# Performance work log

Hardware: AMD Instinct MI355X
Metric: run time of the kernel (lower is better)

The kernel has to match this reference:

```python
import jax, jax.numpy as jnp
import numpy as np

B, S, HID = 2, 2048, 2048
H, KV, D = 16, 8, 128          # query heads, kv heads, head_dim
EPS = 1e-6
THETA = 1000000.0


def setup_inputs() -> dict:
    key = jax.random.key(0)
    ks = jax.random.split(key, 8)
    sc = 0.02
    hidden_states = jax.random.normal(ks[0], (B, S, HID), dtype=jnp.float32)
    Wq = jax.random.normal(ks[1], (HID, H * D), dtype=jnp.float32) * sc
    Wk = jax.random.normal(ks[2], (HID, KV * D), dtype=jnp.float32) * sc
    Wv = jax.random.normal(ks[3], (HID, KV * D), dtype=jnp.float32) * sc
    Wo = jax.random.normal(ks[4], (H * D, HID), dtype=jnp.float32) * sc
    q_norm_w = jnp.ones((D,), dtype=jnp.float32)
    k_norm_w = jnp.ones((D,), dtype=jnp.float32)
    positions = jnp.arange(S, dtype=jnp.int32)
    # causal mask: True = masked (j > i)
    attention_mask = jnp.triu(jnp.ones((S, S), dtype=bool), k=1)
    return {
        "hidden_states": hidden_states, "Wq": Wq, "Wk": Wk, "Wv": Wv,
        "Wo": Wo, "q_norm_w": q_norm_w, "k_norm_w": k_norm_w,
        "positions": positions, "attention_mask": attention_mask,
    }


def _rms_norm(x, w):
    # x: [..., D]; RMSNorm over last dim
    var = jnp.mean(x * x, axis=-1, keepdims=True)
    return x * jax.lax.rsqrt(var + EPS) * w


def _rope(x, positions):
    # x: [B, h, S, D]; standard rotate-half RoPE
    inv_freq = 1.0 / (THETA ** (jnp.arange(0, D, 2, dtype=jnp.float32) / D))
    ang = positions.astype(jnp.float32)[:, None] * inv_freq[None, :]  # [S, D/2]
    cos = jnp.concatenate([jnp.cos(ang), jnp.cos(ang)], axis=-1)      # [S, D]
    sin = jnp.concatenate([jnp.sin(ang), jnp.sin(ang)], axis=-1)
    x1, x2 = x[..., : D // 2], x[..., D // 2:]
    rot = jnp.concatenate([-x2, x1], axis=-1)
    return x * cos + rot * sin


def reference(hidden_states, Wq, Wk, Wv, Wo, q_norm_w, k_norm_w,
              positions, attention_mask):
    b, s, _ = hidden_states.shape
    q = (hidden_states @ Wq).reshape(b, s, H, D).transpose(0, 2, 1, 3)   # [B,H,S,D]
    k = (hidden_states @ Wk).reshape(b, s, KV, D).transpose(0, 2, 1, 3)  # [B,KV,S,D]
    v = (hidden_states @ Wv).reshape(b, s, KV, D).transpose(0, 2, 1, 3)
    q = _rms_norm(q, q_norm_w)
    k = _rms_norm(k, k_norm_w)
    q = _rope(q, positions)
    k = _rope(k, positions)
    # GQA: repeat kv heads
    g = H // KV
    k = jnp.repeat(k, g, axis=1)  # [B,H,S,D]
    v = jnp.repeat(v, g, axis=1)
    scale = 1.0 / np.sqrt(D).astype(np.float32)
    scores = jnp.einsum('bhqd,bhkd->bhqk', q, k) * scale
    scores = jnp.where(attention_mask[None, None, :, :], -jnp.inf, scores)
    attn = jax.nn.softmax(scores, axis=-1)
    out = jnp.einsum('bhqk,bhkd->bhqd', attn, v)
    out = out.transpose(0, 2, 1, 3).reshape(b, s, H * D)
    return out @ Wo
```

## Files before the change

kernel.cpp:

```cpp
#include <hip/hip_runtime.h>
#include <hip/hip_bf16.h>

typedef __hip_bfloat16 bf16;
typedef __attribute__((ext_vector_type(8))) short short8v;
typedef __attribute__((ext_vector_type(4))) float f32x4;

constexpr int nB = 2;
constexpr int nS = 2048;
constexpr int nHID = 2048;
constexpr int nH = 16;
constexpr int nKV = 8;
constexpr int nD = 128;
constexpr int QS = 4096;
constexpr float kEps = 1e-6f;
constexpr float kScale = 0.08838834764831845f;

template <int N>
struct IC {
  static constexpr int value = N;
};

__device__ inline float b2f(unsigned short u) {
  return __uint_as_float(((unsigned)u) << 16);
}
__device__ inline float bf2f(bf16 v) { return __bfloat162float(v); }
__device__ inline short f2bs(float f) {
  bf16 h = __float2bfloat16(f);
  return *reinterpret_cast<short*>(&h);
}
__device__ inline unsigned pack2bf(float a, float b) {
  return ((unsigned)(unsigned short)f2bs(b) << 16) |
         (unsigned)(unsigned short)f2bs(a);
}

__device__ inline void gload_lds16(const bf16* g, bf16* l) {
  __builtin_amdgcn_global_load_lds(
      (const __attribute__((address_space(1))) void*)g,
      (__attribute__((address_space(3))) void*)l, 16, 0, 0);
}

template <int N>
__device__ inline void vwait() {
  asm volatile("s_waitcnt vmcnt(%0)" ::"n"(N) : "memory");
}

__global__ __launch_bounds__(256) void cvt_f32_bf16(
    const float* __restrict__ src, bf16* __restrict__ dst, int n) {
  const int i = (blockIdx.x * 256 + threadIdx.x) * 4;
  if (i >= n) return;
  const float4 v = *reinterpret_cast<const float4*>(src + i);
  ushort4 o;
  o.x = (unsigned short)f2bs(v.x);
  o.y = (unsigned short)f2bs(v.y);
  o.z = (unsigned short)f2bs(v.z);
  o.w = (unsigned short)f2bs(v.w);
  *reinterpret_cast<ushort4*>(dst + i) = o;
}

__global__ __launch_bounds__(64) void rope_table(float2* __restrict__ tab) {
  const int s = blockIdx.x, j = threadIdx.x;
  const float invf = expf(-(float)j * (13.815510557964274f / 64.0f));
  const float ang = (float)s * invf;
  tab[s * 64 + j] = make_float2(cosf(ang), sinf(ang));
}

__global__ __launch_bounds__(256) void transpose_f32_bf16(
    const float* __restrict__ src, bf16* __restrict__ dst, int K, int N) {
  __shared__ float t[32][33];
  const int k0 = blockIdx.y * 32, n0 = blockIdx.x * 32;
  const int c = threadIdx.x & 31, r8 = threadIdx.x >> 5;
#pragma unroll
  for (int i = 0; i < 4; ++i)
    t[r8 + i * 8][c] = src[(size_t)(k0 + r8 + i * 8) * N + n0 + c];
  __syncthreads();
#pragma unroll
  for (int i = 0; i < 4; ++i)
    dst[(size_t)(n0 + r8 + i * 8) * K + k0 + c] =
        __float2bfloat16(t[c][r8 + i * 8]);
}

template <int BM, typename OUT_T>
__global__ __launch_bounds__(512) void gemm_8ph(
    const bf16* __restrict__ A, const bf16* __restrict__ Bt,
    OUT_T* __restrict__ C, int M, int N, int K) {
  constexpr int LA = BM / 128;
  constexpr int LB = 2;
  constexpr int MF = BM / 32;
  constexpr int MFH = MF / 2;
  constexpr int W = 2 * (LA + LB);
  constexpr int LDSB = 2 * BM * 32 + 2 * 256 * 32;
  __shared__ bf16 lds[2 * LDSB];

  const int tid = threadIdx.x;
  const int wave = tid >> 6, lane = tid & 63;
  const int lr = lane & 15, lg = lane >> 4;
  const int wm = wave >> 2, wn = wave & 3;
  const int m0 = blockIdx.y * BM, n0 = blockIdx.x * 256;
  const int srow = tid >> 2, scol = (tid & 3) * 8;

  auto stageA = [&](int t, int kk) {
    bf16* dst = lds + (t & 1) * LDSB + kk * (BM * 32) + wave * 512;
    const bf16* src = A + (size_t)(m0 + srow) * K + t * 64 + kk * 32 + scol;
#pragma unroll
    for (int j = 0; j < LA; ++j)
      gload_lds16(src + (size_t)(j * 128) * K, dst + j * 4096);
  };
  auto stageB = [&](int t, int kk) {
    bf16* dst =
        lds + (t & 1) * LDSB + 2 * BM * 32 + kk * (256 * 32) + wave * 512;
    const bf16* src = Bt + (size_t)(n0 + srow) * K + t * 64 + kk * 32 + scol;
#pragma unroll
    for (int j = 0; j < LB; ++j)
      gload_lds16(src + (size_t)(j * 128) * K, dst + j * 4096);
  };

  f32x4 acc[MF][4];
#pragma unroll
  for (int m = 0; m < MF; ++m)
#pragma unroll
    for (int n = 0; n < 4; ++n) acc[m][n] = (f32x4){0.f, 0.f, 0.f, 0.f};
  short8v bfr[4];

  auto phase = [&](auto WC, int buf, int kk, int mh, auto stageFn) {
    constexpr int WAIT = decltype(WC)::value;
    if constexpr (WAIT >= 0) vwait<WAIT>();
    __builtin_amdgcn_s_barrier();
    asm volatile("" ::: "memory");
    if (mh == 0) {
      const bf16* bb = lds + buf * LDSB + 2 * BM * 32 + kk * (256 * 32);
#pragma unroll
      for (int ni = 0; ni < 4; ++ni)
        bfr[ni] = *reinterpret_cast<const short8v*>(
            bb + (wn * 64 + ni * 16 + lr) * 32 + lg * 8);
    }
    short8v af[MFH];
    const bf16* ab = lds + buf * LDSB + kk * (BM * 32);
#pragma unroll
    for (int ii = 0; ii < MFH; ++ii)
      af[ii] = *reinterpret_cast<const short8v*>(
          ab + (wm * (BM / 2) + (mh * MFH + ii) * 16 + lr) * 32 + lg * 8);
    stageFn();
    asm volatile("s_waitcnt lgkmcnt(0)" ::: "memory");
    __builtin_amdgcn_sched_barrier(0);
    __builtin_amdgcn_s_setprio(1);
#pragma unroll
    for (int ii = 0; ii < MFH; ++ii)
#pragma unroll
      for (int ni = 0; ni < 4; ++ni)
        acc[mh * MFH + ii][ni] = __builtin_amdgcn_mfma_f32_16x16x32_bf16(
            af[ii], bfr[ni], acc[mh * MFH + ii][ni], 0, 0, 0);
    __builtin_amdgcn_s_setprio(0);
  };

  const int NT = K / 64;
  stageA(0, 0);
  stageB(0, 0);
  stageA(0, 1);
  stageB(0, 1);
  stageA(1, 0);
  stageB(1, 0);

  for (int t = 0; t < NT - 1; ++t) {
    const int buf = t & 1;
    phase(IC<W>{}, buf, 0, 0, [&] { stageA(t + 1, 1); });
    phase(IC<-1>{}, buf, 0, 1, [&] { stageB(t + 1, 1); });
    phase(IC<W>{}, buf, 1, 0, [&] {
      if (t < NT - 2) stageA(t + 2, 0);
    });
    phase(IC<-1>{}, buf, 1, 1, [&] {
      if (t < NT - 2) stageB(t + 2, 0);
    });
  }
  {
    const int buf = (NT - 1) & 1;
    phase(IC<LA + LB>{}, buf, 0, 0, [&] {});
    phase(IC<-1>{}, buf, 0, 1, [&] {});
    phase(IC<0>{}, buf, 1, 0, [&] {});
    phase(IC<-1>{}, buf, 1, 1, [&] {});
  }

#pragma unroll
  for (int m = 0; m < MF; ++m)
#pragma unroll
    for (int n = 0; n < 4; ++n)
#pragma unroll
      for (int r = 0; r < 4; ++r) {
        const int row = m0 + wm * (BM / 2) + m * 16 + 4 * lg + r;
        const int col = n0 + wn * 64 + n * 16 + lr;
        if constexpr (sizeof(OUT_T) == 2)
          C[(size_t)row * N + col] = __float2bfloat16(acc[m][n][r]);
        else
          C[(size_t)row * N + col] = acc[m][n][r];
      }
}

__global__ __launch_bounds__(128) void norm_rope_fused(
    bf16* __restrict__ qkv, const float* __restrict__ qw,
    const float* __restrict__ kw, const float2* __restrict__ tab) {
  const int row = blockIdx.x;
  const int head = blockIdx.y;
  const int t = threadIdx.x;
  const int s = row & (nS - 1);
  const bool isQ = head < nH;
  const int col = isQ ? head * nD : 2048 + (head - nH) * nD;
  const float* w = isQ ? qw : kw;
  bf16* xp = qkv + (size_t)row * QS + col;
  const float v = bf2f(xp[t]);
  float ss = v * v;
#pragma unroll
  for (int off = 32; off > 0; off >>= 1) ss += __shfl_xor(ss, off);
  __shared__ float wsum[2];
  __shared__ float buf[nD];
  if ((t & 63) == 0) wsum[t >> 6] = ss;
  __syncthreads();
  const float inv = rsqrtf((wsum[0] + wsum[1]) * (1.0f / nD) + kEps);
  const float nv = v * inv * w[t];
  buf[t] = nv;
  __syncthreads();
  const float partner = buf[t ^ 64];
  const float rot = (t < 64) ? -partner : partner;
  const int j = t & 63;
  const float2 cs = tab[s * 64 + j];
  const float outv = nv * cs.x + rot * cs.y;
  xp[t] = __float2bfloat16(outv);
}

constexpr int BQ = 128, BKT = 64;

__global__ __launch_bounds__(512) void attn_mfma(
    const bf16* __restrict__ QKV, bf16* __restrict__ O) {
  const int l = blockIdx.x;
  const int bh = l & 31;
  const int rr0 = l >> 5;
  const int qb = (rr0 < 8) ? 15 - rr0 : rr0 - 8;
  const int b = bh >> 4, h = bh & 15, kvh = h >> 1;
  const int q0 = qb * BQ;
  const int nt = 2 * qb + 2;
  const int tid = threadIdx.x;
  const int wave = tid >> 6, lane = tid & 63;
  const int lr = lane & 15, lg = lane >> 4;

  __shared__ bf16 Ks[BKT][136];
  __shared__ bf16 Vt[nD][72];
  __shared__ bf16 Pl[8][16][72];

  const bf16* Qbase = QKV + (size_t)b * nS * QS + h * nD;
  const bf16* Kbase = QKV + (size_t)b * nS * QS + 2048 + kvh * nD;
  const bf16* Vbase = QKV + (size_t)b * nS * QS + 3072 + kvh * nD;

  const int krow = tid >> 3, kcc = (tid & 7) * 16;
  const int vkey = tid & 63, vdc = (tid >> 6) * 16;

  short8v kreg[2], vreg[2];
  auto gload = [&](int kt) {
    const bf16* ksrc = Kbase + (size_t)(kt + krow) * QS + kcc;
    const bf16* vsrc = Vbase + (size_t)(kt + vkey) * QS + vdc;
    kreg[0] = *reinterpret_cast<const short8v*>(ksrc);
    kreg[1] = *reinterpret_cast<const short8v*>(ksrc + 8);
    vreg[0] = *reinterpret_cast<const short8v*>(vsrc);
    vreg[1] = *reinterpret_cast<const short8v*>(vsrc + 8);
  };
  auto lwrite = [&]() {
    *reinterpret_cast<short8v*>(&Ks[krow][kcc]) = kreg[0];
    *reinterpret_cast<short8v*>(&Ks[krow][kcc + 8]) = kreg[1];
#pragma unroll
    for (int i = 0; i < 2; ++i)
#pragma unroll
      for (int j = 0; j < 8; ++j)
        *reinterpret_cast<short*>(&Vt[vdc + 8 * i + j][vkey]) = vreg[i][j];
  };

  short8v qf[4];
  {
    const bf16* qrow = Qbase + (size_t)(q0 + 16 * wave + lr) * QS;
#pragma unroll
    for (int dc = 0; dc < 4; ++dc)
      qf[dc] = *reinterpret_cast<const short8v*>(qrow + 32 * dc + 8 * lg);
  }

  f32x4 of[8];
#pragma unroll
  for (int n = 0; n < 8; ++n) of[n] = (f32x4){0.f, 0.f, 0.f, 0.f};
  float m_run = -1e30f, l_run = 0.f;

  gload(0);
  lwrite();
  __syncthreads();

  for (int j = 0; j < nt; ++j) {
    const int kt = j * BKT;
    const bool have_next = (j + 1 < nt);
    if (have_next) gload((j + 1) * BKT);

    f32x4 s[4];
    __builtin_amdgcn_s_setprio(1);
#pragma unroll
    for (int sub = 0; sub < 4; ++sub) {
      f32x4 acc = {0.f, 0.f, 0.f, 0.f};
#pragma unroll
      for (int dc = 0; dc < 4; ++dc) {
        const short8v kf = *reinterpret_cast<const short8v*>(
            &Ks[16 * sub + lr][32 * dc + 8 * lg]);
        acc = __builtin_amdgcn_mfma_f32_16x16x32_bf16(kf, qf[dc], acc, 0, 0, 0);
      }
      s[sub] = acc;
    }
    __builtin_amdgcn_s_setprio(0);

    const bool needMask = (kt + BKT > q0 + 16 * wave);
#pragma unroll
    for (int sub = 0; sub < 4; ++sub)
#pragma unroll
      for (int r = 0; r < 4; ++r) {
        float v = s[sub][r] * kScale;
        if (needMask && (kt + 16 * sub + 4 * lg + r > q0 + 16 * wave + lr))
          v = -1e30f;
        s[sub][r] = v;
      }

    float pmax = -1e30f;
#pragma unroll
    for (int sub = 0; sub < 4; ++sub)
#pragma unroll
      for (int r = 0; r < 4; ++r) pmax = fmaxf(pmax, s[sub][r]);
    pmax = fmaxf(pmax, __shfl_xor(pmax, 16));
    pmax = fmaxf(pmax, __shfl_xor(pmax, 32));

    if (!__all(pmax - m_run <= 8.f)) {
      const float mt = fmaxf(m_run, pmax);
      const float corr = __expf(m_run - mt);
#pragma unroll
      for (int n = 0; n < 8; ++n) of[n] *= corr;
      l_run *= corr;
      m_run = mt;
    }

    float p[4][4];
    float lsum = 0.f;
#pragma unroll
    for (int sub = 0; sub < 4; ++sub)
#pragma unroll
      for (int r = 0; r < 4; ++r) {
        const float e = __expf(s[sub][r] - m_run);
        p[sub][r] = e;
        lsum += e;
      }
    lsum += __shfl_xor(lsum, 16);
    lsum += __shfl_xor(lsum, 32);
    l_run += lsum;

#pragma unroll
    for (int sub = 0; sub < 4; ++sub)
#pragma unroll
      for (int rp = 0; rp < 2; ++rp)
        *reinterpret_cast<unsigned*>(
            &Pl[wave][lr][16 * sub + 4 * lg + 2 * rp]) =
            pack2bf(p[sub][2 * rp], p[sub][2 * rp + 1]);

    __builtin_amdgcn_s_setprio(1);
#pragma unroll
    for (int kk = 0; kk < 2; ++kk) {
      const short8v pb =
          *reinterpret_cast<const short8v*>(&Pl[wave][lr][32 * kk + 8 * lg]);
#pragma unroll
      for (int n = 0; n < 8; ++n) {
        const short8v vf = *reinterpret_cast<const short8v*>(
            &Vt[16 * n + lr][32 * kk + 8 * lg]);
        of[n] = __builtin_amdgcn_mfma_f32_16x16x32_bf16(vf, pb, of[n], 0, 0, 0);
      }
    }
    __builtin_amdgcn_s_setprio(0);

    if (have_next) {
      __syncthreads();
      lwrite();
      __syncthreads();
    }
  }

  {
    const float inv = 1.0f / l_run;
    bf16* orow = O + ((size_t)(b * nS + q0 + 16 * wave + lr)) * (nH * nD) +
                 h * nD + 4 * lg;
#pragma unroll
    for (int n = 0; n < 8; ++n)
#pragma unroll
      for (int rp = 0; rp < 2; ++rp)
        *reinterpret_cast<unsigned*>(orow + 16 * n + 2 * rp) =
            pack2bf(of[n][2 * rp] * inv, of[n][2 * rp + 1] * inv);
  }
}

extern "C" void kernel_launch(void* const* d_in, const int* in_sizes, int n_in,
                              void* d_out, int out_size, void* d_ws,
                              size_t ws_size, hipStream_t stream) {
  const float* hs = (const float*)d_in[0];
  const float* Wq = (const float*)d_in[1];
  const float* Wk = (const float*)d_in[2];
  const float* Wv = (const float*)d_in[3];
  const float* Wo = (const float*)d_in[4];
  const float* qw = (const float*)d_in[5];
  const float* kw = (const float*)d_in[6];

  const int M = nB * nS;
  char* ws = (char*)d_ws;
  size_t off = 0;
  auto alloc = [&](size_t bytes) {
    char* p = ws + off;
    off += bytes;
    return p;
  };
  bf16* hsb = (bf16*)alloc((size_t)M * nHID * 2);
  bf16* att = hsb;
  bf16* qkv = (bf16*)alloc((size_t)M * QS * 2);
  bf16* Wcat = (bf16*)alloc((size_t)QS * nHID * 2);
  bf16* Wot = (bf16*)alloc((size_t)nH * nD * nHID * 2);
  float2* tab = (float2*)alloc((size_t)nS * 64 * 8);
  float* out = (float*)d_out;

  const int nHsElems = M * nHID;
  rope_table<<<dim3(nS), 64, 0, stream>>>(tab);
  cvt_f32_bf16<<<(nHsElems / 4 + 255) / 256, 256, 0, stream>>>(hs, hsb,
                                                               nHsElems);
  transpose_f32_bf16<<<dim3(nH * nD / 32, nHID / 32), 256, 0, stream>>>(
      Wq, Wcat, nHID, nH * nD);
  transpose_f32_bf16<<<dim3(nKV * nD / 32, nHID / 32), 256, 0, stream>>>(
      Wk, Wcat + (size_t)2048 * nHID, nHID, nKV * nD);
  transpose_f32_bf16<<<dim3(nKV * nD / 32, nHID / 32), 256, 0, stream>>>(
      Wv, Wcat + (size_t)3072 * nHID, nHID, nKV * nD);
  transpose_f32_bf16<<<dim3(nHID / 32, nH * nD / 32), 256, 0, stream>>>(
      Wo, Wot, nH * nD, nHID);

  gemm_8ph<256, bf16><<<dim3(QS / 256, M / 256), 512, 0, stream>>>(
      hsb, Wcat, qkv, M, QS, nHID);

  norm_rope_fused<<<dim3(M, nH + nKV), 128, 0, stream>>>(qkv, qw, kw, tab);

  attn_mfma<<<dim3(512), 512, 0, stream>>>(qkv, att);

  gemm_8ph<128, float><<<dim3(nHID / 256, M / 128), 512, 0, stream>>>(
      att, Wot, out, M, nHID, nH * nD);
}
```

Before: 261.7 us.

## Double-buffer K via direct global-to-LDS loads with XOR swizzle; merge weight transposes

The attention kernel now stages K tiles straight from global memory into a double-buffered, XOR-swizzled LDS layout (gload_lds16), so K no longer passes through registers and the next tile's load overlaps the current tile's compute. V is loaded as four rows per thread and written transposed with packed 4-element stores instead of scalar shorts. The four weight-transpose launches are merged into one kernel to cut launch overhead. The cost is more LDS for the second K buffer and an extra vmcnt wait before each barrier. Helper functions gload_lds16 and vwait are assumed to exist in the unshown part of the file.

Result: no change. 265.7 us (+1.5%).

```diff
diff --git a/kernel.cpp b/kernel.cpp
--- a/kernel.cpp
+++ b/kernel.cpp
@@ -64,19 +64,35 @@
   tab[s * 64 + j] = make_float2(cosf(ang), sinf(ang));
 }
 
-__global__ __launch_bounds__(256) void transpose_f32_bf16(
-    const float* __restrict__ src, bf16* __restrict__ dst, int K, int N) {
-  __shared__ float t[32][33];
-  const int k0 = blockIdx.y * 32, n0 = blockIdx.x * 32;
+__global__ __launch_bounds__(256) void transpose_all(
+    const float* __restrict__ Wq, const float* __restrict__ Wk,
+    const float* __restrict__ Wv, const float* __restrict__ Wo,
+    bf16* __restrict__ Wcat, bf16* __restrict__ Wot) {
+  int t = blockIdx.x;
+  const float* src;
+  bf16* dst;
+  int N;
+  if (t < 4096) {
+    src = Wq; dst = Wcat; N = 2048;
+  } else if (t < 6144) {
+    t -= 4096; src = Wk; dst = Wcat + (size_t)2048 * 2048; N = 1024;
+  } else if (t < 8192) {
+    t -= 6144; src = Wv; dst = Wcat + (size_t)3072 * 2048; N = 1024;
+  } else {
+    t -= 8192; src = Wo; dst = Wot; N = 2048;
+  }
+  const int tilesN = N >> 5;
+  const int n0 = (t % tilesN) * 32, k0 = (t / tilesN) * 32;
+  __shared__ float tb[32][33];
   const int c = threadIdx.x & 31, r8 = threadIdx.x >> 5;
 #pragma unroll
   for (int i = 0; i < 4; ++i)
-    t[r8 + i * 8][c] = src[(size_t)(k0 + r8 + i * 8) * N + n0 + c];
+    tb[r8 + i * 8][c] = src[(size_t)(k0 + r8 + i * 8) * N + n0 + c];
   __syncthreads();
 #pragma unroll
   for (int i = 0; i < 4; ++i)
-    dst[(size_t)(n0 + r8 + i * 8) * K + k0 + c] =
-        __float2bfloat16(t[c][r8 + i * 8]);
+    dst[(size_t)(n0 + r8 + i * 8) * 2048 + k0 + c] =
+        __float2bfloat16(tb[c][r8 + i * 8]);
 }
 
 template <int BM, typename OUT_T>
@@ -240,7 +256,7 @@
   const int wave = tid >> 6, lane = tid & 63;
   const int lr = lane & 15, lg = lane >> 4;
 
-  __shared__ bf16 Ks[BKT][136];
+  __shared__ bf16 Ks[2][64 * 128];
   __shared__ bf16 Vt[nD][72];
   __shared__ bf16 Pl[8][16][72];
 
@@ -248,26 +264,32 @@
   const bf16* Kbase = QKV + (size_t)b * nS * QS + 2048 + kvh * nD;
   const bf16* Vbase = QKV + (size_t)b * nS * QS + 3072 + kvh * nD;
 
-  const int krow = tid >> 3, kcc = (tid & 7) * 16;
-  const int vkey = tid & 63, vdc = (tid >> 6) * 16;
-
-  short8v kreg[2], vreg[2];
-  auto gload = [&](int kt) {
-    const bf16* ksrc = Kbase + (size_t)(kt + krow) * QS + kcc;
-    const bf16* vsrc = Vbase + (size_t)(kt + vkey) * QS + vdc;
-    kreg[0] = *reinterpret_cast<const short8v*>(ksrc);
-    kreg[1] = *reinterpret_cast<const short8v*>(ksrc + 8);
-    vreg[0] = *reinterpret_cast<const short8v*>(vsrc);
-    vreg[1] = *reinterpret_cast<const short8v*>(vsrc + 8);
-  };
-  auto lwrite = [&]() {
-    *reinterpret_cast<short8v*>(&Ks[krow][kcc]) = kreg[0];
-    *reinterpret_cast<short8v*>(&Ks[krow][kcc + 8]) = kreg[1];
-#pragma unroll
-    for (int i = 0; i < 2; ++i)
-#pragma unroll
-      for (int j = 0; j < 8; ++j)
-        *reinterpret_cast<short*>(&Vt[vdc + 8 * i + j][vkey]) = vreg[i][j];
+  const int kr = tid >> 4;
+  const int ksw = ((tid & 15) ^ (kr & 7)) * 8;
+  auto stageK = [&](int kt, int buf) {
+    const bf16* src = Kbase + (size_t)(kt + kr) * QS + ksw;
+    gload_lds16(src, &Ks[buf][wave * 512]);
+    gload_lds16(src + (size_t)32 * QS, &Ks[buf][4096 + wave * 512]);
+  };
+
+  const int vk = (tid & 15) * 4, vd = (tid >> 4) * 8;
+  short8v vreg[4];
+  auto vload = [&](int kt) {
+    const bf16* src = Vbase + (size_t)(kt + vk) * QS + vd;
+#pragma unroll
+    for (int i = 0; i < 4; ++i)
+      vreg[i] = *reinterpret_cast<const short8v*>(src + (size_t)i * QS);
+  };
+  auto vwrite = [&]() {
+#pragma unroll
+    for (int j = 0; j < 8; ++j) {
+      ushort4 pk;
+      pk.x = (unsigned short)vreg[0][j];
+      pk.y = (unsigned short)vreg[1][j];
+      pk.z = (unsigned short)vreg[2][j];
+      pk.w = (unsigned short)vreg[3][j];
+      *reinterpret_cast<ushort4*>(&Vt[vd + j][vk]) = pk;
+    }
   };
 
   short8v qf[4];
@@ -283,14 +305,20 @@
   for (int n = 0; n < 8; ++n) of[n] = (f32x4){0.f, 0.f, 0.f, 0.f};
   float m_run = -1e30f, l_run = 0.f;
 
-  gload(0);
-  lwrite();
+  stageK(0, 0);
+  vload(0);
+  vwrite();
+  vwait<0>();
   __syncthreads();
 
+  int cur = 0;
   for (int j = 0; j < nt; ++j) {
     const int kt = j * BKT;
     const bool have_next = (j + 1 < nt);
-    if (have_next) gload((j + 1) * BKT);
+    if (have_next) {
+      stageK(kt + BKT, cur ^ 1);
+      vload(kt + BKT);
+    }
 
     f32x4 s[4];
     __builtin_amdgcn_s_setprio(1);
@@ -300,7 +328,7 @@
 #pragma unroll
       for (int dc = 0; dc < 4; ++dc) {
         const short8v kf = *reinterpret_cast<const short8v*>(
-            &Ks[16 * sub + lr][32 * dc + 8 * lg]);
+            &Ks[cur][(16 * sub + lr) * 128 + (((4 * dc + lg) ^ (lr & 7)) << 3)]);
         acc = __builtin_amdgcn_mfma_f32_16x16x32_bf16(kf, qf[dc], acc, 0, 0, 0);
       }
       s[sub] = acc;
@@ -373,8 +401,10 @@
 
     if (have_next) {
       __syncthreads();
-      lwrite();
+      vwrite();
+      vwait<0>();
       __syncthreads();
+      cur ^= 1;
     }
   }
 
@@ -422,14 +452,7 @@
   rope_table<<<dim3(nS), 64, 0, stream>>>(tab);
   cvt_f32_bf16<<<(nHsElems / 4 + 255) / 256, 256, 0, stream>>>(hs, hsb,
                                                                nHsElems);
-  transpose_f32_bf16<<<dim3(nH * nD / 32, nHID / 32), 256, 0, stream>>>(
-      Wq, Wcat, nHID, nH * nD);
-  transpose_f32_bf16<<<dim3(nKV * nD / 32, nHID / 32), 256, 0, stream>>>(
-      Wk, Wcat + (size_t)2048 * nHID, nHID, nKV * nD);
-  transpose_f32_bf16<<<dim3(nKV * nD / 32, nHID / 32), 256, 0, stream>>>(
-      Wv, Wcat + (size_t)3072 * nHID, nHID, nKV * nD);
-  transpose_f32_bf16<<<dim3(nHID / 32, nH * nD / 32), 256, 0, stream>>>(
-      Wo, Wot, nH * nD, nHID);
+  transpose_all<<<dim3(12288), 256, 0, stream>>>(Wq, Wk, Wv, Wo, Wcat, Wot);
 
   gemm_8ph<256, bf16><<<dim3(QS / 256, M / 256), 512, 0, stream>>>(
       hsb, Wcat, qkv, M, QS, nHID);
```
